# Performance work log

Hardware: AMD Instinct MI355X
Metric: run time of the kernel (lower is better)

## Reference

```python
import jax, jax.numpy as jnp
import numpy as np

B, N, D = 4, 1024, 1024
H, DH = 16, 64
INNER = H * DH
SCALE = DH ** -0.5


def setup_inputs() -> dict:
    key = jax.random.key(0)
    ks = jax.random.split(key, 6)
    std = 0.02
    return {
        "x_re": jax.random.normal(ks[0], (B, N, D), jnp.float32),
        "x_im": jax.random.normal(ks[1], (B, N, D), jnp.float32),
        "wqkv_re": jax.random.normal(ks[2], (INNER, D), jnp.float32) * std,
        "wqkv_im": jax.random.normal(ks[3], (INNER, D), jnp.float32) * std,
        "wout_re": jax.random.normal(ks[4], (D, INNER), jnp.float32) * std,
        "wout_im": jax.random.normal(ks[5], (D, INNER), jnp.float32) * std,
        "bout_re": jnp.zeros((D,), jnp.float32),
        "bout_im": jnp.zeros((D,), jnp.float32),
    }


def reference(x_re, x_im, wqkv_re, wqkv_im, wout_re, wout_im, bout_re, bout_im):
    x = jax.lax.complex(x_re, x_im)                      # [B, N, D] complex64
    Wqkv = jax.lax.complex(wqkv_re, wqkv_im)             # [INNER, D]
    Wout = jax.lax.complex(wout_re, wout_im)             # [D, INNER]
    bout = jax.lax.complex(bout_re, bout_im)             # [D]

    # shared q=k=v projection: w = x @ Wqkv^T, split into heads
    w = jnp.einsum('bnd,ed->bne', x, Wqkv)               # [B, N, INNER]
    w = w.reshape(B, N, H, DH).transpose(0, 2, 1, 3)     # [B, H, N, DH]

    # complex dot-product scores: w @ w^H
    dots = jnp.einsum('bhnd,bhmd->bhnm', w, jnp.conj(w)) * SCALE

    # magnitude-softmax with phase reconstruction (polar(softmax(|z|), angle(z)))
    mag = jnp.abs(dots)                                   # [B, H, N, N] float32
    a = jax.nn.softmax(mag, axis=-1)
    # unit phase factor z/|z|; torch.polar(r, angle(0)=0) -> r, so use 1 where mag==0
    unit = jnp.where(mag > 0, dots, 1.0 + 0.0j) / jnp.where(mag > 0, mag, 1.0)
    attn = a.astype(jnp.complex64) * unit                 # complex attention weights

    out = jnp.einsum('bhnm,bhmd->bhnd', attn, w)          # [B, H, N, DH]
    out = out.transpose(0, 2, 1, 3).reshape(B, N, INNER)  # [B, N, INNER]
    out = jnp.einsum('bne,de->bnd', out, Wout) + bout     # [B, N, D]
    return out
```

## Files before the change

kernel.cpp:

```cpp
#include <hip/hip_runtime.h>
#include <hip/hip_bf16.h>

#define Bn 4
#define Nn 1024
#define Dn 1024
#define Hn 16
#define DHn 64
#define INNERn 1024
#define SCALEf 0.125f

typedef unsigned short u16;
using bf16x8 = __attribute__((ext_vector_type(8))) short;
using f32x4  = __attribute__((ext_vector_type(4))) float;

__device__ __forceinline__ u16 f2bf(float f) {
    __hip_bfloat16 h = __float2bfloat16(f);
    return *(u16*)&h;
}
__device__ __forceinline__ float bf2f(u16 h) {
    union { unsigned int u; float f; } cv;
    cv.u = ((unsigned int)h) << 16;
    return cv.f;
}
__device__ __forceinline__ bf16x8 bfneg(bf16x8 v) {
    bf16x8 r;
#pragma unroll
    for (int j = 0; j < 8; ++j) r[j] = (short)(v[j] ^ (short)0x8000);
    return r;
}

#define MFMA16(acc, a, b) acc = __builtin_amdgcn_mfma_f32_16x16x32_bf16(a, b, acc, 0, 0, 0)

__global__ __launch_bounds__(256) void split6(
    const float* __restrict__ x_re, const float* __restrict__ x_im,
    const float* __restrict__ wq_re, const float* __restrict__ wq_im,
    const float* __restrict__ wo_re, const float* __restrict__ wo_im,
    u16* __restrict__ xh_re, u16* __restrict__ xl_re,
    u16* __restrict__ xh_im, u16* __restrict__ xl_im,
    u16* __restrict__ wqh_re, u16* __restrict__ wql_re,
    u16* __restrict__ wqh_im, u16* __restrict__ wql_im,
    u16* __restrict__ woh_re, u16* __restrict__ wol_re,
    u16* __restrict__ woh_im, u16* __restrict__ wol_im)
{
    const float* in; u16* hi; u16* lo; size_t n;
    switch (blockIdx.y) {
        case 0:  in = x_re;  hi = xh_re;  lo = xl_re;  n = 4194304; break;
        case 1:  in = x_im;  hi = xh_im;  lo = xl_im;  n = 4194304; break;
        case 2:  in = wq_re; hi = wqh_re; lo = wql_re; n = 1048576; break;
        case 3:  in = wq_im; hi = wqh_im; lo = wql_im; n = 1048576; break;
        case 4:  in = wo_re; hi = woh_re; lo = wol_re; n = 1048576; break;
        default: in = wo_im; hi = woh_im; lo = wol_im; n = 1048576; break;
    }
    size_t i = ((size_t)blockIdx.x * 256 + threadIdx.x) * 8;
    if (i >= n) return;
    float4 f0 = *(const float4*)(in + i);
    float4 f1 = *(const float4*)(in + i + 4);
    float v[8] = {f0.x, f0.y, f0.z, f0.w, f1.x, f1.y, f1.z, f1.w};
    bf16x8 h8, l8;
#pragma unroll
    for (int j = 0; j < 8; ++j) {
        u16 hh = f2bf(v[j]);
        h8[j] = (short)hh;
        l8[j] = (short)f2bf(v[j] - bf2f(hh));
    }
    *(bf16x8*)(hi + i) = h8;
    *(bf16x8*)(lo + i) = l8;
}

__global__ __launch_bounds__(256) void gemm_qkv_mfma(
    const u16* __restrict__ xh_re, const u16* __restrict__ xl_re,
    const u16* __restrict__ xh_im, const u16* __restrict__ xl_im,
    const u16* __restrict__ qh_re, const u16* __restrict__ ql_re,
    const u16* __restrict__ qh_im, const u16* __restrict__ ql_im,
    u16* __restrict__ w_re16, u16* __restrict__ w_im16)
{
    const int K = Dn;
    __shared__ __align__(16) u16 Ahr[64][40], Alr[64][40], Ahi[64][40], Ali[64][40];
    __shared__ __align__(16) u16 Bhr[128][40], Blr[128][40], Bhi[128][40], Bli[128][40];

    int t    = threadIdx.x;
    int lane = t & 63;
    int wv   = t >> 6;
    int lq   = lane & 15, qd = lane >> 4;
    int wr   = wv >> 1,   wc = wv & 1;

    int m0 = blockIdx.y * 64;
    int e0 = blockIdx.x * 128;

    int ar = t >> 2, ac = (t & 3) * 8;
    int br = t >> 1, bc = (t & 1) * 16;

    const u16* pA0 = xh_re + (size_t)(m0 + ar) * K + ac;
    const u16* pA1 = xl_re + (size_t)(m0 + ar) * K + ac;
    const u16* pA2 = xh_im + (size_t)(m0 + ar) * K + ac;
    const u16* pA3 = xl_im + (size_t)(m0 + ar) * K + ac;
    const u16* pB0 = qh_re + (size_t)(e0 + br) * K + bc;
    const u16* pB1 = ql_re + (size_t)(e0 + br) * K + bc;
    const u16* pB2 = qh_im + (size_t)(e0 + br) * K + bc;
    const u16* pB3 = ql_im + (size_t)(e0 + br) * K + bc;

    f32x4 accR[2][4], accI[2][4];
#pragma unroll
    for (int i = 0; i < 2; ++i)
#pragma unroll
        for (int j = 0; j < 4; ++j) { accR[i][j] = (f32x4)0.f; accI[i][j] = (f32x4)0.f; }

    for (int k0 = 0; k0 < K; k0 += 32) {
        bf16x8 va0 = *(const bf16x8*)(pA0 + k0);
        bf16x8 va1 = *(const bf16x8*)(pA1 + k0);
        bf16x8 va2 = *(const bf16x8*)(pA2 + k0);
        bf16x8 va3 = *(const bf16x8*)(pA3 + k0);
        bf16x8 vb0a = *(const bf16x8*)(pB0 + k0), vb0b = *(const bf16x8*)(pB0 + k0 + 8);
        bf16x8 vb1a = *(const bf16x8*)(pB1 + k0), vb1b = *(const bf16x8*)(pB1 + k0 + 8);
        bf16x8 vb2a = *(const bf16x8*)(pB2 + k0), vb2b = *(const bf16x8*)(pB2 + k0 + 8);
        bf16x8 vb3a = *(const bf16x8*)(pB3 + k0), vb3b = *(const bf16x8*)(pB3 + k0 + 8);
        __syncthreads();
        *(bf16x8*)&Ahr[ar][ac] = va0;
        *(bf16x8*)&Alr[ar][ac] = va1;
        *(bf16x8*)&Ahi[ar][ac] = va2;
        *(bf16x8*)&Ali[ar][ac] = va3;
        *(bf16x8*)&Bhr[br][bc] = vb0a; *(bf16x8*)&Bhr[br][bc+8] = vb0b;
        *(bf16x8*)&Blr[br][bc] = vb1a; *(bf16x8*)&Blr[br][bc+8] = vb1b;
        *(bf16x8*)&Bhi[br][bc] = vb2a; *(bf16x8*)&Bhi[br][bc+8] = vb2b;
        *(bf16x8*)&Bli[br][bc] = vb3a; *(bf16x8*)&Bli[br][bc+8] = vb3b;
        __syncthreads();

        bf16x8 Arh[2], Arl[2], Aih[2], Ail[2], Anh[2], Anl[2];
#pragma unroll
        for (int rf = 0; rf < 2; ++rf) {
            int row = wr*32 + rf*16 + lq;
            Arh[rf] = *(const bf16x8*)&Ahr[row][qd*8];
            Arl[rf] = *(const bf16x8*)&Alr[row][qd*8];
            Aih[rf] = *(const bf16x8*)&Ahi[row][qd*8];
            Ail[rf] = *(const bf16x8*)&Ali[row][qd*8];
            Anh[rf] = bfneg(Aih[rf]);
            Anl[rf] = bfneg(Ail[rf]);
        }
#pragma unroll
        for (int cf = 0; cf < 4; ++cf) {
            int col = wc*64 + cf*16 + lq;
            bf16x8 Brh = *(const bf16x8*)&Bhr[col][qd*8];
            bf16x8 Brl = *(const bf16x8*)&Blr[col][qd*8];
            bf16x8 Bih = *(const bf16x8*)&Bhi[col][qd*8];
            bf16x8 Bil = *(const bf16x8*)&Bli[col][qd*8];
#pragma unroll
            for (int rf = 0; rf < 2; ++rf) {
                MFMA16(accR[rf][cf], Arh[rf], Brh);
                MFMA16(accR[rf][cf], Arh[rf], Brl);
                MFMA16(accR[rf][cf], Arl[rf], Brh);
                MFMA16(accR[rf][cf], Anh[rf], Bih);
                MFMA16(accR[rf][cf], Anh[rf], Bil);
                MFMA16(accR[rf][cf], Anl[rf], Bih);
                MFMA16(accI[rf][cf], Arh[rf], Bih);
                MFMA16(accI[rf][cf], Arh[rf], Bil);
                MFMA16(accI[rf][cf], Arl[rf], Bih);
                MFMA16(accI[rf][cf], Aih[rf], Brh);
                MFMA16(accI[rf][cf], Aih[rf], Brl);
                MFMA16(accI[rf][cf], Ail[rf], Brh);
            }
        }
    }

#pragma unroll
    for (int rf = 0; rf < 2; ++rf)
#pragma unroll
        for (int cf = 0; cf < 4; ++cf)
#pragma unroll
            for (int p = 0; p < 4; ++p) {
                int m = m0 + wr*32 + rf*16 + qd*4 + p;
                int e = e0 + wc*64 + cf*16 + lq;
                int b = m >> 10, n = m & 1023;
                int h = e >> 6,  dh = e & 63;
                size_t idx = ((size_t)(b*Hn + h) * Nn + n) * DHn + dh;
                w_re16[idx] = f2bf(accR[rf][cf][p]);
                w_im16[idx] = f2bf(accI[rf][cf][p]);
            }
}

__global__ __launch_bounds__(256, 4) void attn_mfma(
    const u16* __restrict__ w_re16, const u16* __restrict__ w_im16,
    u16* __restrict__ ah_re, u16* __restrict__ al_re,
    u16* __restrict__ ah_im, u16* __restrict__ al_im)
{
    __shared__ __align__(16) u16 Kr[32][72], Ki[32][72];
    __shared__ __align__(16) u16 Ktr[64][40], Kti[64][40];
    __shared__ __align__(16) u16 Pr[64][40], Pi[64][40];

    int t    = threadIdx.x;
    int lane = t & 63;
    int wv   = t >> 6;
    int lq   = lane & 15;
    int qd   = lane >> 4;
    int r0   = wv * 16;

    int n0 = blockIdx.x * 64;
    int bh = blockIdx.y;
    int b  = bh >> 4, h = bh & 15;
    const u16* wr = w_re16 + (size_t)bh * (Nn*DHn);
    const u16* wi = w_im16 + (size_t)bh * (Nn*DHn);

    bf16x8 qfr[2], qfi[2], qfn[2];
    {
        const u16* qr = wr + (size_t)(n0 + r0 + lq) * DHn + qd*8;
        const u16* qi = wi + (size_t)(n0 + r0 + lq) * DHn + qd*8;
#pragma unroll
        for (int c = 0; c < 2; ++c) {
            qfr[c] = *(const bf16x8*)(qr + c*32);
            qfi[c] = *(const bf16x8*)(qi + c*32);
            qfn[c] = bfneg(qfr[c]);
        }
    }

    float rm[4], rl[4];
#pragma unroll
    for (int p = 0; p < 4; ++p) { rm[p] = -1e30f; rl[p] = 0.f; }
    f32x4 Ore[4], Oim[4];
#pragma unroll
    for (int d = 0; d < 4; ++d) { Ore[d] = (f32x4)0.f; Oim[d] = (f32x4)0.f; }

    int sm = t >> 3, sdc = (t & 7) * 8;
    int gdh = t & 63, gmc = t >> 6;

    for (int kt = 0; kt < Nn/32; ++kt) {
        __syncthreads();
        {
            const u16* pr = wr + (size_t)(kt*32 + sm) * DHn + sdc;
            const u16* pi = wi + (size_t)(kt*32 + sm) * DHn + sdc;
            *(bf16x8*)&Kr[sm][sdc] = *(const bf16x8*)pr;
            *(bf16x8*)&Ki[sm][sdc] = *(const bf16x8*)pi;
        }
        {
            const u16* gr = wr + (size_t)(kt*32 + gmc*8) * DHn + gdh;
            const u16* gi = wi + (size_t)(kt*32 + gmc*8) * DHn + gdh;
            bf16x8 tr, ti;
#pragma unroll
            for (int j = 0; j < 8; ++j) {
                tr[j] = (short)gr[(size_t)j * DHn];
                ti[j] = (short)gi[(size_t)j * DHn];
            }
            *(bf16x8*)&Ktr[gdh][gmc*8] = tr;
            *(bf16x8*)&Kti[gdh][gmc*8] = ti;
        }
        __syncthreads();

        float sre[2][4], sim[2][4], mag[2][4];
#pragma unroll
        for (int ct = 0; ct < 2; ++ct) {
            bf16x8 bkr[2], bki[2];
#pragma unroll
            for (int c = 0; c < 2; ++c) {
                bkr[c] = *(const bf16x8*)&Kr[ct*16 + lq][c*32 + qd*8];
                bki[c] = *(const bf16x8*)&Ki[ct*16 + lq][c*32 + qd*8];
            }
            f32x4 are = (f32x4)0.f, aim = (f32x4)0.f;
            __builtin_amdgcn_s_setprio(1);
            are = __builtin_amdgcn_mfma_f32_16x16x32_bf16(qfr[0], bkr[0], are, 0,0,0);
            are = __builtin_amdgcn_mfma_f32_16x16x32_bf16(qfi[0], bki[0], are, 0,0,0);
            are = __builtin_amdgcn_mfma_f32_16x16x32_bf16(qfr[1], bkr[1], are, 0,0,0);
            are = __builtin_amdgcn_mfma_f32_16x16x32_bf16(qfi[1], bki[1], are, 0,0,0);
            aim = __builtin_amdgcn_mfma_f32_16x16x32_bf16(qfi[0], bkr[0], aim, 0,0,0);
            aim = __builtin_amdgcn_mfma_f32_16x16x32_bf16(qfn[0], bki[0], aim, 0,0,0);
            aim = __builtin_amdgcn_mfma_f32_16x16x32_bf16(qfi[1], bkr[1], aim, 0,0,0);
            aim = __builtin_amdgcn_mfma_f32_16x16x32_bf16(qfn[1], bki[1], aim, 0,0,0);
            __builtin_amdgcn_s_setprio(0);
#pragma unroll
            for (int p = 0; p < 4; ++p) {
                float r = are[p] * SCALEf;
                float i = aim[p] * SCALEf;
                sre[ct][p] = r; sim[ct][p] = i;
                mag[ct][p] = sqrtf(r*r + i*i);
            }
        }

        float alpha[4];
#pragma unroll
        for (int p = 0; p < 4; ++p) {
            float pm = fmaxf(mag[0][p], mag[1][p]);
            pm = fmaxf(pm, __shfl_xor(pm, 1));
            pm = fmaxf(pm, __shfl_xor(pm, 2));
            pm = fmaxf(pm, __shfl_xor(pm, 4));
            pm = fmaxf(pm, __shfl_xor(pm, 8));
            float mnew = fmaxf(rm[p], pm);
            alpha[p] = __expf(rm[p] - mnew);
            rm[p] = mnew;
        }
#pragma unroll
        for (int p = 0; p < 4; ++p) {
            float s = 0.f;
            int q = r0 + qd*4 + p;
#pragma unroll
            for (int ct = 0; ct < 2; ++ct) {
                float mg = mag[ct][p];
                float e = __expf(mg - rm[p]);
                s += e;
                float cr, ci;
                if (mg > 0.f) {
                    float f = e * __builtin_amdgcn_rcpf(mg);
                    cr = sre[ct][p] * f; ci = sim[ct][p] * f;
                } else { cr = e; ci = 0.f; }
                Pr[q][ct*16 + lq] = f2bf(cr);
                Pi[q][ct*16 + lq] = f2bf(ci);
            }
            s += __shfl_xor(s, 1);
            s += __shfl_xor(s, 2);
            s += __shfl_xor(s, 4);
            s += __shfl_xor(s, 8);
            rl[p] = rl[p]*alpha[p] + s;
        }

        if (alpha[0] != 1.f || alpha[1] != 1.f || alpha[2] != 1.f || alpha[3] != 1.f) {
#pragma unroll
            for (int d = 0; d < 4; ++d)
#pragma unroll
                for (int p = 0; p < 4; ++p) {
                    Ore[d][p] *= alpha[p];
                    Oim[d][p] *= alpha[p];
                }
        }

        bf16x8 par = *(const bf16x8*)&Pr[r0 + lq][qd*8];
        bf16x8 pai = *(const bf16x8*)&Pi[r0 + lq][qd*8];
        bf16x8 pan = bfneg(pai);
        __builtin_amdgcn_s_setprio(1);
#pragma unroll
        for (int d = 0; d < 4; ++d) {
            bf16x8 fr = *(const bf16x8*)&Ktr[d*16 + lq][qd*8];
            bf16x8 fi = *(const bf16x8*)&Kti[d*16 + lq][qd*8];
            Ore[d] = __builtin_amdgcn_mfma_f32_16x16x32_bf16(par, fr, Ore[d], 0,0,0);
            Ore[d] = __builtin_amdgcn_mfma_f32_16x16x32_bf16(pan, fi, Ore[d], 0,0,0);
            Oim[d] = __builtin_amdgcn_mfma_f32_16x16x32_bf16(par, fi, Oim[d], 0,0,0);
            Oim[d] = __builtin_amdgcn_mfma_f32_16x16x32_bf16(pai, fr, Oim[d], 0,0,0);
        }
        __builtin_amdgcn_s_setprio(0);
    }

#pragma unroll
    for (int p = 0; p < 4; ++p) {
        float inv = 1.f / rl[p];
        int n = n0 + r0 + qd*4 + p;
#pragma unroll
        for (int d = 0; d < 4; ++d) {
            int dh = d*16 + lq;
            size_t idx = ((size_t)b*Nn + n) * INNERn + h*DHn + dh;
            float vr = Ore[d][p] * inv;
            float vi = Oim[d][p] * inv;
            u16 hr = f2bf(vr);
            u16 hm = f2bf(vi);
            ah_re[idx] = hr; al_re[idx] = f2bf(vr - bf2f(hr));
            ah_im[idx] = hm; al_im[idx] = f2bf(vi - bf2f(hm));
        }
    }
}

__global__ __launch_bounds__(256) void gemm_out_mfma(
    const u16* __restrict__ ah_re, const u16* __restrict__ al_re,
    const u16* __restrict__ ah_im, const u16* __restrict__ al_im,
    const u16* __restrict__ oh_re, const u16* __restrict__ ol_re,
    const u16* __restrict__ oh_im, const u16* __restrict__ ol_im,
    const float* __restrict__ b_re, float* __restrict__ out)
{
    const int K = INNERn;
    __shared__ __align__(16) u16 Ahr[64][40], Alr[64][40], Ahi[64][40], Ali[64][40];
    __shared__ __align__(16) u16 Bhr[128][40], Blr[128][40], Bhi[128][40], Bli[128][40];

    int t    = threadIdx.x;
    int lane = t & 63;
    int wv   = t >> 6;
    int lq   = lane & 15, qd = lane >> 4;
    int wr   = wv >> 1,   wc = wv & 1;

    int m0 = blockIdx.y * 64;
    int d0 = blockIdx.x * 128;

    int ar = t >> 2, ac = (t & 3) * 8;
    int br = t >> 1, bc = (t & 1) * 16;

    const u16* pA0 = ah_re + (size_t)(m0 + ar) * K + ac;
    const u16* pA1 = al_re + (size_t)(m0 + ar) * K + ac;
    const u16* pA2 = ah_im + (size_t)(m0 + ar) * K + ac;
    const u16* pA3 = al_im + (size_t)(m0 + ar) * K + ac;
    const u16* pB0 = oh_re + (size_t)(d0 + br) * K + bc;
    const u16* pB1 = ol_re + (size_t)(d0 + br) * K + bc;
    const u16* pB2 = oh_im + (size_t)(d0 + br) * K + bc;
    const u16* pB3 = ol_im + (size_t)(d0 + br) * K + bc;

    f32x4 accR[2][4];
#pragma unroll
    for (int i = 0; i < 2; ++i)
#pragma unroll
        for (int j = 0; j < 4; ++j) accR[i][j] = (f32x4)0.f;

    for (int k0 = 0; k0 < K; k0 += 32) {
        bf16x8 va0 = *(const bf16x8*)(pA0 + k0);
        bf16x8 va1 = *(const bf16x8*)(pA1 + k0);
        bf16x8 va2 = *(const bf16x8*)(pA2 + k0);
        bf16x8 va3 = *(const bf16x8*)(pA3 + k0);
        bf16x8 vb0a = *(const bf16x8*)(pB0 + k0), vb0b = *(const bf16x8*)(pB0 + k0 + 8);
        bf16x8 vb1a = *(const bf16x8*)(pB1 + k0), vb1b = *(const bf16x8*)(pB1 + k0 + 8);
        bf16x8 vb2a = *(const bf16x8*)(pB2 + k0), vb2b = *(const bf16x8*)(pB2 + k0 + 8);
        bf16x8 vb3a = *(const bf16x8*)(pB3 + k0), vb3b = *(const bf16x8*)(pB3 + k0 + 8);
        __syncthreads();
        *(bf16x8*)&Ahr[ar][ac] = va0;
        *(bf16x8*)&Alr[ar][ac] = va1;
        *(bf16x8*)&Ahi[ar][ac] = va2;
        *(bf16x8*)&Ali[ar][ac] = va3;
        *(bf16x8*)&Bhr[br][bc] = vb0a; *(bf16x8*)&Bhr[br][bc+8] = vb0b;
        *(bf16x8*)&Blr[br][bc] = vb1a; *(bf16x8*)&Blr[br][bc+8] = vb1b;
        *(bf16x8*)&Bhi[br][bc] = vb2a; *(bf16x8*)&Bhi[br][bc+8] = vb2b;
        *(bf16x8*)&Bli[br][bc] = vb3a; *(bf16x8*)&Bli[br][bc+8] = vb3b;
        __syncthreads();

        bf16x8 Arh[2], Arl[2], Anh[2], Anl[2];
#pragma unroll
        for (int rf = 0; rf < 2; ++rf) {
            int row = wr*32 + rf*16 + lq;
            Arh[rf] = *(const bf16x8*)&Ahr[row][qd*8];
            Arl[rf] = *(const bf16x8*)&Alr[row][qd*8];
            Anh[rf] = bfneg(*(const bf16x8*)&Ahi[row][qd*8]);
            Anl[rf] = bfneg(*(const bf16x8*)&Ali[row][qd*8]);
        }
#pragma unroll
        for (int cf = 0; cf < 4; ++cf) {
            int col = wc*64 + cf*16 + lq;
            bf16x8 Brh = *(const bf16x8*)&Bhr[col][qd*8];
            bf16x8 Brl = *(const bf16x8*)&Blr[col][qd*8];
            bf16x8 Bih = *(const bf16x8*)&Bhi[col][qd*8];
            bf16x8 Bil = *(const bf16x8*)&Bli[col][qd*8];
#pragma unroll
            for (int rf = 0; rf < 2; ++rf) {
                MFMA16(accR[rf][cf], Arh[rf], Brh);
                MFMA16(accR[rf][cf], Arh[rf], Brl);
                MFMA16(accR[rf][cf], Arl[rf], Brh);
                MFMA16(accR[rf][cf], Anh[rf], Bih);
                MFMA16(accR[rf][cf], Anh[rf], Bil);
                MFMA16(accR[rf][cf], Anl[rf], Bih);
            }
        }
    }

#pragma unroll
    for (int rf = 0; rf < 2; ++rf)
#pragma unroll
        for (int cf = 0; cf < 4; ++cf)
#pragma unroll
            for (int p = 0; p < 4; ++p) {
                int m = m0 + wr*32 + rf*16 + qd*4 + p;
                int d = d0 + wc*64 + cf*16 + lq;
                out[(size_t)m * Dn + d] = accR[rf][cf][p] + b_re[d];
            }
}

extern "C" void kernel_launch(void* const* d_in, const int* in_sizes, int n_in,
                              void* d_out, int out_size, void* d_ws, size_t ws_size,
                              hipStream_t stream) {
    const float* x_re  = (const float*)d_in[0];
    const float* x_im  = (const float*)d_in[1];
    const float* wq_re = (const float*)d_in[2];
    const float* wq_im = (const float*)d_in[3];
    const float* wo_re = (const float*)d_in[4];
    const float* wo_im = (const float*)d_in[5];
    const float* bo_re = (const float*)d_in[6];

    const size_t M4 = (size_t)Bn * Nn * INNERn;
    const size_t M1 = (size_t)INNERn * Dn;

    u16* ws = (u16*)d_ws;
    u16* xh_re = ws;
    u16* xl_re = ws + M4;
    u16* xh_im = ws + 2*M4;
    u16* xl_im = ws + 3*M4;
    u16* wqh_re = ws + 4*M4;
    u16* wql_re = wqh_re + M1;
    u16* wqh_im = wql_re + M1;
    u16* wql_im = wqh_im + M1;
    u16* woh_re = wql_im + M1;
    u16* wol_re = woh_re + M1;
    u16* woh_im = wol_re + M1;
    u16* wol_im = woh_im + M1;
    u16* w_re16 = wol_im + M1;
    u16* w_im16 = w_re16 + M4;
    u16* ah_re = xh_re;
    u16* al_re = xl_re;
    u16* ah_im = xh_im;
    u16* al_im = xl_im;

    {
        dim3 grid(2048, 6);
        split6<<<grid, 256, 0, stream>>>(x_re, x_im, wq_re, wq_im, wo_re, wo_im,
            xh_re, xl_re, xh_im, xl_im,
            wqh_re, wql_re, wqh_im, wql_im,
            woh_re, wol_re, woh_im, wol_im);
    }
    {
        dim3 grid(INNERn / 128, (Bn * Nn) / 64);
        gemm_qkv_mfma<<<grid, 256, 0, stream>>>(
            xh_re, xl_re, xh_im, xl_im,
            wqh_re, wql_re, wqh_im, wql_im,
            w_re16, w_im16);
    }
    {
        dim3 grid(Nn / 64, Bn * Hn);
        attn_mfma<<<grid, 256, 0, stream>>>(w_re16, w_im16,
                                            ah_re, al_re, ah_im, al_im);
    }
    {
        dim3 grid(Dn / 128, (Bn * Nn) / 64);
        gemm_out_mfma<<<grid, 256, 0, stream>>>(
            ah_re, al_re, ah_im, al_im,
            woh_re, wol_re, woh_im, wol_im,
            bo_re, (float*)d_out);
    }
}
```

Measured before the change: 423.0 us.

## Shrink attention blocks to 32 queries and read K rows directly from global

```diff
diff --git a/kernel.cpp b/kernel.cpp
--- a/kernel.cpp
+++ b/kernel.cpp
@@ -177,14 +177,13 @@
             }
 }
 
-__global__ __launch_bounds__(256, 4) void attn_mfma(
+__global__ __launch_bounds__(128, 4) void attn_mfma(
     const u16* __restrict__ w_re16, const u16* __restrict__ w_im16,
     u16* __restrict__ ah_re, u16* __restrict__ al_re,
     u16* __restrict__ ah_im, u16* __restrict__ al_im)
 {
-    __shared__ __align__(16) u16 Kr[32][72], Ki[32][72];
     __shared__ __align__(16) u16 Ktr[64][40], Kti[64][40];
-    __shared__ __align__(16) u16 Pr[64][40], Pi[64][40];
+    __shared__ __align__(16) u16 Pr[32][40], Pi[32][40];
 
     int t    = threadIdx.x;
     int lane = t & 63;
@@ -193,7 +192,7 @@
     int qd   = lane >> 4;
     int r0   = wv * 16;
 
-    int n0 = blockIdx.x * 64;
+    int n0 = blockIdx.x * 32;
     int bh = blockIdx.y;
     int b  = bh >> 4, h = bh & 15;
     const u16* wr = w_re16 + (size_t)bh * (Nn*DHn);
@@ -218,39 +217,40 @@
 #pragma unroll
     for (int d = 0; d < 4; ++d) { Ore[d] = (f32x4)0.f; Oim[d] = (f32x4)0.f; }
 
-    int sm = t >> 3, sdc = (t & 7) * 8;
-    int gdh = t & 63, gmc = t >> 6;
+    int gdh = t & 63;
+    int gmh = t >> 6;
 
     for (int kt = 0; kt < Nn/32; ++kt) {
         __syncthreads();
         {
-            const u16* pr = wr + (size_t)(kt*32 + sm) * DHn + sdc;
-            const u16* pi = wi + (size_t)(kt*32 + sm) * DHn + sdc;
-            *(bf16x8*)&Kr[sm][sdc] = *(const bf16x8*)pr;
-            *(bf16x8*)&Ki[sm][sdc] = *(const bf16x8*)pi;
-        }
-        {
-            const u16* gr = wr + (size_t)(kt*32 + gmc*8) * DHn + gdh;
-            const u16* gi = wi + (size_t)(kt*32 + gmc*8) * DHn + gdh;
-            bf16x8 tr, ti;
+            const u16* gr = wr + (size_t)(kt*32 + gmh*16) * DHn + gdh;
+            const u16* gi = wi + (size_t)(kt*32 + gmh*16) * DHn + gdh;
+            bf16x8 t0, t1, u0, u1;
 #pragma unroll
             for (int j = 0; j < 8; ++j) {
-                tr[j] = (short)gr[(size_t)j * DHn];
-                ti[j] = (short)gi[(size_t)j * DHn];
-            }
-            *(bf16x8*)&Ktr[gdh][gmc*8] = tr;
-            *(bf16x8*)&Kti[gdh][gmc*8] = ti;
+                t0[j] = (short)gr[(size_t)j * DHn];
+                t1[j] = (short)gr[(size_t)(8 + j) * DHn];
+                u0[j] = (short)gi[(size_t)j * DHn];
+                u1[j] = (short)gi[(size_t)(8 + j) * DHn];
+            }
+            *(bf16x8*)&Ktr[gdh][gmh*16]     = t0;
+            *(bf16x8*)&Ktr[gdh][gmh*16 + 8] = t1;
+            *(bf16x8*)&Kti[gdh][gmh*16]     = u0;
+            *(bf16x8*)&Kti[gdh][gmh*16 + 8] = u1;
         }
         __syncthreads();
 
         float sre[2][4], sim[2][4], mag[2][4];
+        const u16* kbr = wr + (size_t)(kt*32) * DHn;
+        const u16* kbi = wi + (size_t)(kt*32) * DHn;
 #pragma unroll
         for (int ct = 0; ct < 2; ++ct) {
+            size_t roff = (size_t)(ct*16 + lq) * DHn + qd*8;
             bf16x8 bkr[2], bki[2];
 #pragma unroll
             for (int c = 0; c < 2; ++c) {
-                bkr[c] = *(const bf16x8*)&Kr[ct*16 + lq][c*32 + qd*8];
-                bki[c] = *(const bf16x8*)&Ki[ct*16 + lq][c*32 + qd*8];
+                bkr[c] = *(const bf16x8*)(kbr + roff + c*32);
+                bki[c] = *(const bf16x8*)(kbi + roff + c*32);
             }
             f32x4 are = (f32x4)0.f, aim = (f32x4)0.f;
             __builtin_amdgcn_s_setprio(1);
@@ -499,8 +499,8 @@
             w_re16, w_im16);
     }
     {
-        dim3 grid(Nn / 64, Bn * Hn);
-        attn_mfma<<<grid, 256, 0, stream>>>(w_re16, w_im16,
+        dim3 grid(Nn / 32, Bn * Hn);
+        attn_mfma<<<grid, 128, 0, stream>>>(w_re16, w_im16,
                                             ah_re, al_re, ah_im, al_im);
     }
     {
```

Result: slower. 450.7 us (+6.6%).
